# Kernel optimization log

Hardware: AMD Instinct MI355X
Metric: run time of the kernel (lower is better)

## Reference

```python
import jax, jax.numpy as jnp
import numpy as np

STEP, LEAK = 16, 32
KS = STEP + LEAK          # kernel_size = 48
FODEP = KS                # forced depression window
SYNAPSES, NEURONS = 64, 256
IC, OC = 1, 10
DENSE = 0.5
THETA = DENSE * SYNAPSES * IC   # 32.0
BIAS = 0.5
BATCH, TIME = 16, 512


def setup_inputs() -> dict:
    key = jax.random.key(0)
    k1, k2 = jax.random.split(key)
    # binary input spikes, density 0.2
    input_spikes = (jax.random.uniform(k1, (BATCH, IC, SYNAPSES, TIME)) < 0.2).astype(jnp.float32)
    # weight ~ Exponential(rate=1/w_init=2).sample().clip(0,1), mean 0.5
    u = jax.random.uniform(k2, (OC * NEURONS, IC * SYNAPSES), minval=1e-6, maxval=1.0)
    weight = jnp.clip(-0.5 * jnp.log(u), 0.0, 1.0)
    return {"input_spikes": input_spikes, "weight": weight}


def _step_fire_leak_kernel(weight):
    # kernel[o, i, t] = max(0, min(t/step, -(t - w*step)/leak + w)), flipped on t
    t = jnp.arange(KS, dtype=weight.dtype)
    t_spike = t / STEP                                        # rising edge
    t_leak = -(t - weight[..., None] * STEP) / LEAK + weight[..., None]  # decaying edge
    kernel = jnp.maximum(jnp.zeros((), weight.dtype), jnp.minimum(t_spike, t_leak))
    return kernel[..., ::-1]


def _forward(input_spikes, weight):
    B, C, S, T = input_spikes.shape
    x = input_spikes.reshape(B, C * S, T)
    kernel = _step_fire_leak_kernel(weight)                   # [OC*N, IC*S, KS]
    # conv1d with padding = kernel_size on both sides -> T' = T + KS + 1
    pot = jax.lax.conv_general_dilated(
        x, kernel, window_strides=(1,), padding=[(KS, KS)],
        dimension_numbers=("NCH", "OIH", "NCH"))
    Tp = pot.shape[-1]
    pot = pot.reshape(B, OC, NEURONS, Tp) + BIAS * THETA      # unsupervised bias path

    # winner-takes-all scan over time with per-(batch, neuron) depression counter
    pot_t = pot.transpose(3, 0, 2, 1)                         # [T', B, N, OC]
    dep0 = jnp.zeros((B, NEURONS, OC), jnp.int32)

    def step_fn(dep, p):
        masked = jnp.where(dep == 0, p, jnp.zeros((), p.dtype))
        winner = jnp.argmax(masked, axis=-1)                  # [B, N]
        wpot = jnp.take_along_axis(masked, winner[..., None], axis=-1)[..., 0]
        spike = (wpot > THETA).astype(p.dtype)                # [B, N]
        w_t = jax.nn.one_hot(winner, OC, dtype=p.dtype) * spike[..., None]
        dep = jnp.clip(dep + spike.astype(jnp.int32)[..., None] * FODEP - 1, 0, FODEP - 1)
        return dep, w_t

    _, winners = jax.lax.scan(step_fn, dep0, pot_t)           # [T', B, N, OC]
    return winners.transpose(1, 3, 2, 0)                      # [B, OC, N, T'] float


def reference(input_spikes, weight):
    return _forward(input_spikes, weight)
```

## Files before the change

kernel.cpp:

```cpp
#include <hip/hip_runtime.h>

#define B_   16
#define OC_  10
#define N_   256
#define O_   2560
#define S_   64
#define T_   512
#define KS_  48
#define TP_  561
#define TT   24
#define WROW 72

#define NOC   160
#define XROWS 624

#define SCH    16
#define CPITCH 572

using i32x4 = __attribute__((ext_vector_type(4))) int;

__global__ void prep_all(const float* __restrict__ x, const float* __restrict__ w,
                         unsigned char* __restrict__ xb, signed char* __restrict__ Bg) {
    if (blockIdx.x < 512) {
#pragma unroll
        for (int it = 0; it < 4; ++it) {
            int idx = blockIdx.x * 256 + threadIdx.x + it * 131072;
            int t = idx & 511;
            int bi = idx >> 9;
            int i = bi & 63, b = bi >> 6;
            xb[((size_t)(b * 512 + t) << 6) + i] = (x[idx] != 0.0f) ? 1 : 0;
        }
    } else {
        int base = (blockIdx.x - 512) * 256 + threadIdx.x;
#pragma unroll
        for (int it = 0; it < 16; ++it) {
            int idx = base + it * 491520;
            int i = idx & 63;
            int oj = idx >> 6;
            int j = oj % KS_, o = oj / KS_;
            float wv = w[(o << 6) + i];
            float rise = (float)j * 0.0625f;
            float leak = -((float)j - wv * 16.0f) * 0.03125f + wv;
            float kv   = fmaxf(0.0f, fminf(rise, leak));
            int q  = (int)lrintf(kv * 4194304.0f);
            int d0 = ((q + 128) & 255) - 128;
            int q1 = (q - d0) >> 8;
            int d1 = ((q1 + 128) & 255) - 128;
            int d2 = (q1 - d1) >> 8;
            int oc = o >> 4, ol = o & 15;
            int jm = j & 15, jh = j >> 4;
            int pos = jm * 3 + jh;
            size_t bse = (((size_t)(oc * KS_ + pos) * 48) + ol) * 64 + i;
            Bg[bse]            = (signed char)d0;
            Bg[bse + 16 * 64]  = (signed char)d1;
            Bg[bse + 32 * 64]  = (signed char)d2;
        }
    }
}

__global__ __launch_bounds__(256, 2) void gemm_i8(
    const unsigned char* __restrict__ xb,
    const signed char*  __restrict__ Bg,
    float* __restrict__ pot)
{
    __shared__ __align__(16) unsigned char xT[XROWS * 64];

    const int tid  = threadIdx.x;
    const int lane = tid & 63;
    const int wave = tid >> 6;
    const int oc = blockIdx.x;
    const int b  = blockIdx.y;
    const int lrow = lane & 15;
    const int quad = lane >> 4;
    const int tw = wave * 144;

    const signed char* Bgb = Bg + (size_t)oc * (KS_ * 48 * 64)
                           + lrow * 64 + quad * 16;

    for (int z = tid; z < 112 * 4; z += 256) {
        int zi = z >> 2, p = z & 3;
        int r = (zi < 49) ? zi : (561 + zi - 49);
        *(i32x4*)(xT + r * 64 + p * 16) = (i32x4){0, 0, 0, 0};
    }
    const unsigned char* xbb = xb + ((size_t)b << 15);
    for (int q = tid; q < 2048; q += 256) {
        i32x4 v = *(const i32x4*)(xbb + q * 16);
        int t = q >> 2, p = q & 3;
        int r = 49 + t;
        *(i32x4*)(xT + r * 64 + ((p ^ ((r >> 1) & 3)) << 4)) = v;
    }

    i32x4 acc[9][3];
#pragma unroll
    for (int mi = 0; mi < 9; ++mi)
#pragma unroll
        for (int f = 0; f < 3; ++f)
            acc[mi][f] = (i32x4){0, 0, 0, 0};

    i32x4 af[11], bfA[9], bfB[9];

#pragma unroll
    for (int jh = 0; jh < 3; ++jh)
#pragma unroll
        for (int f = 0; f < 3; ++f)
            bfA[jh * 3 + f] = *(const i32x4*)(Bgb + jh * 3072 + f * 1024);

    __syncthreads();

    {
        const int rb0 = tw + 16 + lrow;
        const int ca0 = ((quad ^ ((rb0 >> 1) & 3)) << 4);
#pragma unroll
        for (int k = 0; k < 11; ++k)
            af[k] = *(const i32x4*)(xT + (rb0 + k * 16) * 64 + ca0);
    }

#define MF(bfC, mi, jh, f)                                                    \
    acc[mi][f] = __builtin_amdgcn_mfma_i32_16x16x64_i8(                       \
        af[(mi) + 2 - (jh)], bfC[(jh) * 3 + (f)], acc[mi][f], 0, 0, 0)

#define PAIR(bfC, m0)                                                         \
    MF(bfC, m0, 0, 0); MF(bfC, m0, 0, 1); MF(bfC, m0, 0, 2);                  \
    MF(bfC, (m0)+1, 0, 0); MF(bfC, (m0)+1, 0, 1); MF(bfC, (m0)+1, 0, 2);      \
    MF(bfC, m0, 1, 0); MF(bfC, m0, 1, 1); MF(bfC, m0, 1, 2);                  \
    MF(bfC, (m0)+1, 1, 0); MF(bfC, (m0)+1, 1, 1); MF(bfC, (m0)+1, 1, 2);      \
    MF(bfC, m0, 2, 0); MF(bfC, m0, 2, 1); MF(bfC, m0, 2, 2);                  \
    MF(bfC, (m0)+1, 2, 0); MF(bfC, (m0)+1, 2, 1); MF(bfC, (m0)+1, 2, 2);

#define PAIR9(bfC)                                                            \
    MF(bfC, 8, 0, 0); MF(bfC, 8, 0, 1); MF(bfC, 8, 0, 2);                     \
    MF(bfC, 8, 1, 0); MF(bfC, 8, 1, 1); MF(bfC, 8, 1, 2);                     \
    MF(bfC, 8, 2, 0); MF(bfC, 8, 2, 1); MF(bfC, 8, 2, 2);

#define LDA_(row) (*(const i32x4*)(xT + (row) * 64 + coffN))
#define LDB_(jh, f) (*(const i32x4*)(Bgb + (tn3 + (jh)) * 3072 + (f) * 1024))

#define TLOC(T, bfC, bfN) {                                                   \
        const int rbn   = tw + 16 - ((T) + 1) + lrow;    \
        const int coffN = ((quad ^ ((rbn >> 1) & 3)) << 4);                   \
        const int tn3   = (((T) + 1) & 15) * 3;         \
        __builtin_amdgcn_s_setprio(1);                                        \
        PAIR(bfC, 0)                                                          \
        af[0] = LDA_(rbn);        af[1] = LDA_(rbn + 16);                     \
        bfN[0] = LDB_(0, 0); bfN[1] = LDB_(0, 1); bfN[2] = LDB_(0, 2);        \
        PAIR(bfC, 2)                                                          \
        af[2] = LDA_(rbn + 32);   af[3] = LDA_(rbn + 48);                     \
        bfN[3] = LDB_(1, 0); bfN[4] = LDB_(1, 1); bfN[5] = LDB_(1, 2);        \
        PAIR(bfC, 4)                                                          \
        af[4] = LDA_(rbn + 64);   af[5] = LDA_(rbn + 80);                     \
        bfN[6] = LDB_(2, 0); bfN[7] = LDB_(2, 1); bfN[8] = LDB_(2, 2);        \
        PAIR(bfC, 6)                                                          \
        af[6] = LDA_(rbn + 96);   af[7] = LDA_(rbn + 112);                    \
        PAIR9(bfC)                                                            \
        af[8] = LDA_(rbn + 128);  af[9] = LDA_(rbn + 144);                    \
        af[10] = LDA_(rbn + 160);                                             \
        __builtin_amdgcn_s_setprio(0);                                        \
    }

    for (int tp = 0; tp < 8; ++tp) {
        TLOC(2 * tp,     bfA, bfB)
        TLOC(2 * tp + 1, bfB, bfA)
    }

#undef MF
#undef PAIR
#undef PAIR9
#undef LDA_
#undef LDB_
#undef TLOC

    const size_t potb = (size_t)b * TP_;
#pragma unroll
    for (int mi = 0; mi < 9; ++mi) {
#pragma unroll
        for (int r = 0; r < 4; ++r) {
            int t = tw + mi * 16 + quad * 4 + r;
            if (t < TP_) {
                double pq = ((double)acc[mi][0][r]
                           + 256.0   * (double)acc[mi][1][r]
                           + 65536.0 * (double)acc[mi][2][r])
                          * (1.0 / 4194304.0);
                pot[(potb + t) * O_ + oc * 16 + lrow] = (float)pq;
            }
        }
    }
}

__global__ __launch_bounds__(1024) void scan_fused(
    const float* __restrict__ pot,
    float* __restrict__ out)
{
    __shared__ unsigned char codeW[SCH * CPITCH];
    __shared__ unsigned char ocW[SCH * CPITCH];

    const int tid = threadIdx.x;
    const int nc = blockIdx.x;
    const int b  = blockIdx.y;
    const int n0 = nc * SCH;

    for (int pair = tid; pair < TP_ * SCH; pair += 1024) {
        int t = pair >> 4, nl = pair & 15;
        const float* p = pot + ((size_t)(b * TP_ + t)) * O_ + n0 + nl;
        float best = p[0]; int bo = 0;
#pragma unroll
        for (int ch = 1; ch < OC_; ++ch) {
            float v = p[ch * N_];
            if (v > best) { best = v; bo = ch; }
        }
        codeW[nl * CPITCH + t] =
            ((best + 16.0f) > 32.0f) ? (unsigned char)(bo + 1) : (unsigned char)0;
        ocW[nl * CPITCH + t] = 0;
    }
    __syncthreads();

    {
        const int wv = tid >> 6;
        const int ln = tid & 63;
        const unsigned char* c = &codeW[wv * CPITCH];
        unsigned char* o = &ocW[wv * CPITCH];
        int t = 0;
        while (t < TP_) {
            int tt = t + ln;
            unsigned char v = (tt < TP_) ? c[tt] : (unsigned char)0;
            unsigned long long mask = __ballot(v != 0);
            if (mask == 0ULL) { t += 64; continue; }
            int k = (int)__builtin_ctzll(mask);
            if (ln == k) o[t + k] = v;
            t += k + KS_;
        }
    }
    __syncthreads();

    float* ob = out + (((size_t)b * OC_) * N_ + n0) * TP_;
    for (int idx = tid; idx < OC_ * SCH * TP_; idx += 1024) {
        int r = idx / TP_;
        int t = idx - r * TP_;
        int ch = r >> 4, nl = r & 15;
        float v = (ocW[nl * CPITCH + t] == (unsigned char)(ch + 1)) ? 1.0f : 0.0f;
        ob[((size_t)ch * N_ + nl) * TP_ + t] = v;
    }
}

__global__ void transpose_w(const float* __restrict__ w, float* __restrict__ wT) {
    int idx = blockIdx.x * 256 + threadIdx.x;
    if (idx >= O_ * S_) return;
    int o = idx >> 6, i = idx & 63;
    wT[i * O_ + o] = w[idx];
}

__global__ __launch_bounds__(256) void conv_kernel(
    const float* __restrict__ x, const float* __restrict__ wT,
    float* __restrict__ pot)
{
    const int b  = blockIdx.y;
    const int t0 = blockIdx.z * TT;
    const int o  = blockIdx.x * 256 + threadIdx.x;

    __shared__ __align__(16) float xsh[S_][WROW];
    for (int idx = threadIdx.x; idx < S_ * WROW; idx += 256) {
        int i = idx / WROW, m = idx - i * WROW;
        int t = t0 - KS_ + m;
        float v = 0.0f;
        if (t >= 0 && t < T_) v = x[(b * S_ + i) * T_ + t];
        xsh[i][m] = v;
    }
    __syncthreads();

    float acch[TT], accl[TT];
#pragma unroll
    for (int tl = 0; tl < TT; ++tl) { acch[tl] = 0.0f; accl[tl] = 0.0f; }

    for (int i = 0; i < S_; ++i) {
        float xw[WROW];
#pragma unroll
        for (int w4 = 0; w4 < WROW / 4; ++w4) {
            const float4 v = *reinterpret_cast<const float4*>(&xsh[i][w4 * 4]);
            xw[w4 * 4 + 0] = v.x; xw[w4 * 4 + 1] = v.y;
            xw[w4 * 4 + 2] = v.z; xw[w4 * 4 + 3] = v.w;
        }
        const float wv = wT[i * O_ + o];
#pragma unroll
        for (int j = 1; j < KS_; ++j) {
            float rise = (float)j * 0.0625f;
            float leak = -((float)j - wv * 16.0f) * 0.03125f + wv;
            float kv   = fmaxf(0.0f, fminf(rise, leak));
            float khi  = rintf(kv * 4096.0f) * 2.44140625e-4f;
            float klo  = kv - khi;
#pragma unroll
            for (int tl = 0; tl < TT; ++tl) {
                float xv = xw[tl + (KS_ - 1) - j];
                acch[tl] = fmaf(xv, khi, acch[tl]);
                accl[tl] = fmaf(xv, klo, accl[tl]);
            }
        }
    }
#pragma unroll
    for (int tl = 0; tl < TT; ++tl) {
        int t = t0 + tl;
        if (t < TP_) pot[((size_t)b * TP_ + t) * O_ + o] = acch[tl] + accl[tl];
    }
}

__global__ void scan_prep(const float* __restrict__ pot, unsigned char* __restrict__ code) {
    int idx = blockIdx.x * 256 + threadIdx.x;
    if (idx >= B_ * TP_ * N_) return;
    int n  = idx & (N_ - 1);
    int bt = idx >> 8;
    const float* p = pot + (size_t)bt * O_ + n;
    float best = p[0]; int bo = 0;
#pragma unroll
    for (int oc = 1; oc < OC_; ++oc) {
        float v = p[oc * N_];
        if (v > best) { best = v; bo = oc; }
    }
    code[idx] = ((best + 16.0f) > 32.0f) ? (unsigned char)(bo + 1) : (unsigned char)0;
}

__global__ void scan_run(const unsigned char* __restrict__ code, float* __restrict__ out) {
    int idx = blockIdx.x * 256 + threadIdx.x;
    if (idx >= B_ * N_) return;
    int b = idx >> 8, n = idx & 255;
    const unsigned char* c = code + (size_t)b * TP_ * N_ + n;
    int t = 0;
    while (t < TP_) {
        unsigned char buf[KS_];
#pragma unroll
        for (int k = 0; k < KS_; ++k) {
            int tt = t + k;
            buf[k] = (tt < TP_) ? c[(size_t)tt * N_] : (unsigned char)0;
        }
        int adv = KS_;
#pragma unroll
        for (int k = 0; k < KS_; ++k) {
            if (buf[k]) {
                out[(((size_t)b * OC_ + (buf[k] - 1)) * N_ + n) * TP_ + (t + k)] = 1.0f;
                adv = k + KS_;
                break;
            }
        }
        t += adv;
    }
}

extern "C" void kernel_launch(void* const* d_in, const int* in_sizes, int n_in,
                              void* d_out, int out_size, void* d_ws, size_t ws_size,
                              hipStream_t stream) {
    const float* x = (const float*)d_in[0];
    const float* w = (const float*)d_in[1];
    float* out = (float*)d_out;

    char* ws = (char*)d_ws;
    const size_t szX = (size_t)B_ * T_ * S_;
    const size_t szB = (size_t)NOC * KS_ * 48 * 64;
    const size_t szP = (size_t)B_ * TP_ * O_ * 4;
    const size_t szC = (size_t)B_ * TP_ * N_;
    const size_t need = szX + szB + szP + szC;

    if (ws_size >= need) {
        unsigned char* xb  = (unsigned char*)ws;
        signed char* Bg    = (signed char*)(ws + szX);
        float* pot         = (float*)(ws + szX + szB);

        prep_all<<<2432, 256, 0, stream>>>(x, w, xb, Bg);
        gemm_i8<<<dim3(NOC, B_), 256, 0, stream>>>(xb, Bg, pot);
        scan_fused<<<dim3(N_ / SCH, B_), 1024, 0, stream>>>(pot, out);
    } else {
        size_t pot_bytes  = (size_t)B_ * TP_ * O_ * sizeof(float);
        size_t code_bytes = (size_t)B_ * TP_ * N_;
        float* pot = (float*)ws;
        unsigned char* code = (unsigned char*)(ws + pot_bytes);
        float* wT = (float*)(ws + pot_bytes + code_bytes);

        hipMemsetAsync(d_out, 0, (size_t)out_size * sizeof(float), stream);
        transpose_w<<<(O_ * S_ + 255) / 256, 256, 0, stream>>>(w, wT);
        conv_kernel<<<dim3(O_ / 256, B_, (TP_ + TT - 1) / TT), 256, 0, stream>>>(x, wT, pot);
        scan_prep<<<(B_ * TP_ * N_ + 255) / 256, 256, 0, stream>>>(pot, code);
        scan_run<<<(B_ * N_ + 255) / 256, 256, 0, stream>>>(code, out);
    }
}
```

Baseline: 245.0 us.

## Fuse int8 conv GEMM with winner-take-all scan, dropping the global potential buffer

```diff
diff --git a/kernel.cpp b/kernel.cpp
--- a/kernel.cpp
+++ b/kernel.cpp
@@ -11,9 +11,7 @@
 #define TT   24
 #define WROW 72
 
-#define NOC   160
 #define XROWS 624
-
 #define SCH    16
 #define CPITCH 572
 
@@ -58,32 +56,39 @@
     }
 }
 
-__global__ __launch_bounds__(256, 2) void gemm_i8(
+__global__ __launch_bounds__(512, 2) void gemm_scan(
     const unsigned char* __restrict__ xb,
     const signed char*  __restrict__ Bg,
-    float* __restrict__ pot)
+    float* __restrict__ out)
 {
     __shared__ __align__(16) unsigned char xT[XROWS * 64];
+    __shared__ float         keyB[2][576 * 16];
+    __shared__ unsigned char codeB[2][576 * 16];
+    __shared__ unsigned char codeW[SCH * CPITCH];
+    __shared__ unsigned char ocW[SCH * CPITCH];
 
     const int tid  = threadIdx.x;
     const int lane = tid & 63;
     const int wave = tid >> 6;
-    const int oc = blockIdx.x;
+    const int tq   = wave >> 1;
+    const int chh  = wave & 1;
+    const int nc = blockIdx.x;
     const int b  = blockIdx.y;
     const int lrow = lane & 15;
     const int quad = lane >> 4;
-    const int tw = wave * 144;
-
-    const signed char* Bgb = Bg + (size_t)oc * (KS_ * 48 * 64)
-                           + lrow * 64 + quad * 16;
-
-    for (int z = tid; z < 112 * 4; z += 256) {
+    const int tw = tq * 144;
+
+    const size_t SL = (size_t)KS_ * 48 * 64;
+    const signed char* Bcur = Bg + (size_t)(chh * 80 + nc) * SL
+                            + lrow * 64 + quad * 16;
+
+    for (int z = tid; z < 112 * 4; z += 512) {
         int zi = z >> 2, p = z & 3;
         int r = (zi < 49) ? zi : (561 + zi - 49);
         *(i32x4*)(xT + r * 64 + p * 16) = (i32x4){0, 0, 0, 0};
     }
     const unsigned char* xbb = xb + ((size_t)b << 15);
-    for (int q = tid; q < 2048; q += 256) {
+    for (int q = tid; q < 2048; q += 512) {
         i32x4 v = *(const i32x4*)(xbb + q * 16);
         int t = q >> 2, p = q & 3;
         int r = 49 + t;
@@ -91,19 +96,13 @@
     }
 
     i32x4 acc[9][3];
-#pragma unroll
-    for (int mi = 0; mi < 9; ++mi)
+    i32x4 af[11], bfA[9], bfB[9];
+
+#pragma unroll
+    for (int jh = 0; jh < 3; ++jh)
 #pragma unroll
         for (int f = 0; f < 3; ++f)
-            acc[mi][f] = (i32x4){0, 0, 0, 0};
-
-    i32x4 af[11], bfA[9], bfB[9];
-
-#pragma unroll
-    for (int jh = 0; jh < 3; ++jh)
-#pragma unroll
-        for (int f = 0; f < 3; ++f)
-            bfA[jh * 3 + f] = *(const i32x4*)(Bgb + jh * 3072 + f * 1024);
+            bfA[jh * 3 + f] = *(const i32x4*)(Bcur + jh * 3072 + f * 1024);
 
     __syncthreads();
 
@@ -133,22 +132,22 @@
     MF(bfC, 8, 2, 0); MF(bfC, 8, 2, 1); MF(bfC, 8, 2, 2);
 
 #define LDA_(row) (*(const i32x4*)(xT + (row) * 64 + coffN))
-#define LDB_(jh, f) (*(const i32x4*)(Bgb + (tn3 + (jh)) * 3072 + (f) * 1024))
-
-#define TLOC(T, bfC, bfN) {                                                   \
-        const int rbn   = tw + 16 - ((T) + 1) + lrow;    \
+#define LDB_(BP, jh, f) (*(const i32x4*)((BP) + (tn3 + (jh)) * 3072 + (f) * 1024))
+
+#define TLOC(T, bfC, bfN, BP) {                                               \
+        const int rbn   = tw + 16 - (((T) + 1) & 15) + lrow;                  \
         const int coffN = ((quad ^ ((rbn >> 1) & 3)) << 4);                   \
-        const int tn3   = (((T) + 1) & 15) * 3;         \
+        const int tn3   = (((T) + 1) & 15) * 3;                               \
         __builtin_amdgcn_s_setprio(1);                                        \
         PAIR(bfC, 0)                                                          \
         af[0] = LDA_(rbn);        af[1] = LDA_(rbn + 16);                     \
-        bfN[0] = LDB_(0, 0); bfN[1] = LDB_(0, 1); bfN[2] = LDB_(0, 2);        \
+        bfN[0] = LDB_(BP, 0, 0); bfN[1] = LDB_(BP, 0, 1); bfN[2] = LDB_(BP, 0, 2); \
         PAIR(bfC, 2)                                                          \
         af[2] = LDA_(rbn + 32);   af[3] = LDA_(rbn + 48);                     \
-        bfN[3] = LDB_(1, 0); bfN[4] = LDB_(1, 1); bfN[5] = LDB_(1, 2);        \
+        bfN[3] = LDB_(BP, 1, 0); bfN[4] = LDB_(BP, 1, 1); bfN[5] = LDB_(BP, 1, 2); \
         PAIR(bfC, 4)                                                          \
         af[4] = LDA_(rbn + 64);   af[5] = LDA_(rbn + 80);                     \
-        bfN[6] = LDB_(2, 0); bfN[7] = LDB_(2, 1); bfN[8] = LDB_(2, 2);        \
+        bfN[6] = LDB_(BP, 2, 0); bfN[7] = LDB_(BP, 2, 1); bfN[8] = LDB_(BP, 2, 2); \
         PAIR(bfC, 6)                                                          \
         af[6] = LDA_(rbn + 96);   af[7] = LDA_(rbn + 112);                    \
         PAIR9(bfC)                                                            \
@@ -157,9 +156,44 @@
         __builtin_amdgcn_s_setprio(0);                                        \
     }
 
-    for (int tp = 0; tp < 8; ++tp) {
-        TLOC(2 * tp,     bfA, bfB)
-        TLOC(2 * tp + 1, bfB, bfA)
+    for (int c = 0; c < 5; ++c) {
+        const signed char* Bnxt = (c == 4) ? Bcur : (Bcur + 16 * SL);
+
+#pragma unroll
+        for (int mi = 0; mi < 9; ++mi)
+#pragma unroll
+            for (int f = 0; f < 3; ++f)
+                acc[mi][f] = (i32x4){0, 0, 0, 0};
+
+        for (int tp = 0; tp < 7; ++tp) {
+            TLOC(2 * tp,     bfA, bfB, Bcur)
+            TLOC(2 * tp + 1, bfB, bfA, Bcur)
+        }
+        TLOC(14, bfA, bfB, Bcur)
+        TLOC(15, bfB, bfA, Bnxt)
+
+        {
+            const unsigned char cv = (unsigned char)(chh * 5 + c + 1);
+            const int cc = c;
+#pragma unroll
+            for (int mi = 0; mi < 9; ++mi) {
+#pragma unroll
+                for (int r = 0; r < 4; ++r) {
+                    int t = tw + mi * 16 + quad * 4 + r;
+                    float pq = (float)(((double)acc[mi][0][r]
+                               + 256.0   * (double)acc[mi][1][r]
+                               + 65536.0 * (double)acc[mi][2][r])
+                              * (1.0 / 4194304.0));
+                    int ix = t * 16 + lrow;
+                    if (cc == 0) {
+                        keyB[chh][ix] = pq; codeB[chh][ix] = cv;
+                    } else if (pq > keyB[chh][ix]) {
+                        keyB[chh][ix] = pq; codeB[chh][ix] = cv;
+                    }
+                }
+            }
+        }
+        Bcur = Bnxt;
     }
 
 #undef MF
@@ -169,70 +203,42 @@
 #undef LDB_
 #undef TLOC
 
-    const size_t potb = (size_t)b * TP_;
-#pragma unroll
-    for (int mi = 0; mi < 9; ++mi) {
-#pragma unroll
-        for (int r = 0; r < 4; ++r) {
-            int t = tw + mi * 16 + quad * 4 + r;
-            if (t < TP_) {
-                double pq = ((double)acc[mi][0][r]
-                           + 256.0   * (double)acc[mi][1][r]
-                           + 65536.0 * (double)acc[mi][2][r])
-                          * (1.0 / 4194304.0);
-                pot[(potb + t) * O_ + oc * 16 + lrow] = (float)pq;
+    __syncthreads();
+
+    for (int ix = tid; ix < 576 * 16; ix += 512) {
+        int t = ix >> 4, nl = ix & 15;
+        if (t >= TP_) continue;
+        float f0 = keyB[0][ix];
+        float f1 = keyB[1][ix];
+        float best = f0;
+        unsigned char cd = codeB[0][ix];
+        if (f1 > f0) { best = f1; cd = codeB[1][ix]; }
+        codeW[nl * CPITCH + t] = ((best + 16.0f) > 32.0f) ? cd : (unsigned char)0;
+        ocW[nl * CPITCH + t] = 0;
+    }
+    __syncthreads();
+
+    {
+        const int ln = tid & 63;
+        for (int nsel = wave; nsel < SCH; nsel += 8) {
+            const unsigned char* cp = &codeW[nsel * CPITCH];
+            unsigned char* op = &ocW[nsel * CPITCH];
+            int t = 0;
+            while (t < TP_) {
+                int tt = t + ln;
+                unsigned char v = (tt < TP_) ? cp[tt] : (unsigned char)0;
+                unsigned long long mask = __ballot(v != 0);
+                if (mask == 0ULL) { t += 64; continue; }
+                int k = (int)__builtin_ctzll(mask);
+                if (ln == k) op[t + k] = v;
+                t += k + KS_;
             }
         }
     }
-}
-
-__global__ __launch_bounds__(1024) void scan_fused(
-    const float* __restrict__ pot,
-    float* __restrict__ out)
-{
-    __shared__ unsigned char codeW[SCH * CPITCH];
-    __shared__ unsigned char ocW[SCH * CPITCH];
-
-    const int tid = threadIdx.x;
-    const int nc = blockIdx.x;
-    const int b  = blockIdx.y;
-    const int n0 = nc * SCH;
-
-    for (int pair = tid; pair < TP_ * SCH; pair += 1024) {
-        int t = pair >> 4, nl = pair & 15;
-        const float* p = pot + ((size_t)(b * TP_ + t)) * O_ + n0 + nl;
-        float best = p[0]; int bo = 0;
-#pragma unroll
-        for (int ch = 1; ch < OC_; ++ch) {
-            float v = p[ch * N_];
-            if (v > best) { best = v; bo = ch; }
-        }
-        codeW[nl * CPITCH + t] =
-            ((best + 16.0f) > 32.0f) ? (unsigned char)(bo + 1) : (unsigned char)0;
-        ocW[nl * CPITCH + t] = 0;
-    }
-    __syncthreads();
-
-    {
-        const int wv = tid >> 6;
-        const int ln = tid & 63;
-        const unsigned char* c = &codeW[wv * CPITCH];
-        unsigned char* o = &ocW[wv * CPITCH];
-        int t = 0;
-        while (t < TP_) {
-            int tt = t + ln;
-            unsigned char v = (tt < TP_) ? c[tt] : (unsigned char)0;
-            unsigned long long mask = __ballot(v != 0);
-            if (mask == 0ULL) { t += 64; continue; }
-            int k = (int)__builtin_ctzll(mask);
-            if (ln == k) o[t + k] = v;
-            t += k + KS_;
-        }
-    }
-    __syncthreads();
-
-    float* ob = out + (((size_t)b * OC_) * N_ + n0) * TP_;
-    for (int idx = tid; idx < OC_ * SCH * TP_; idx += 1024) {
+    __syncthreads();
+
+    float* ob = out + (((size_t)b * OC_) * N_ + nc * SCH) * TP_;
+    for (int idx = tid; idx < OC_ * SCH * TP_; idx += 512) {
         int r = idx / TP_;
         int t = idx - r * TP_;
         int ch = r >> 4, nl = r & 15;
@@ -351,19 +357,15 @@
 
     char* ws = (char*)d_ws;
     const size_t szX = (size_t)B_ * T_ * S_;
-    const size_t szB = (size_t)NOC * KS_ * 48 * 64;
-    const size_t szP = (size_t)B_ * TP_ * O_ * 4;
-    const size_t szC = (size_t)B_ * TP_ * N_;
-    const size_t need = szX + szB + szP + szC;
+    const size_t szB = (size_t)160 * KS_ * 48 * 64;
+    const size_t need = szX + szB;
 
     if (ws_size >= need) {
         unsigned char* xb  = (unsigned char*)ws;
         signed char* Bg    = (signed char*)(ws + szX);
-        float* pot         = (float*)(ws + szX + szB);
 
         prep_all<<<2432, 256, 0, stream>>>(x, w, xb, Bg);
-        gemm_i8<<<dim3(NOC, B_), 256, 0, stream>>>(xb, Bg, pot);
-        scan_fused<<<dim3(N_ / SCH, B_), 1024, 0, stream>>>(pot, out);
+        gemm_scan<<<dim3(16, 16), 512, 0, stream>>>(xb, Bg, out);
     } else {
         size_t pot_bytes  = (size_t)B_ * TP_ * O_ * sizeof(float);
         size_t code_bytes = (size_t)B_ * TP_ * N_;
```

Measured after the change: 237.1 us. 1.03x faster.
